# Kernel optimization log

Hardware: AMD Instinct MI355X
Metric: run time of the kernel (lower is better)

The kernel has to match this reference:

```python
import jax, jax.numpy as jnp
import numpy as np

B, C, H, W = 8, 64, 64, 64
CQ = C // 8  # query/key channels


def setup_inputs() -> dict:
    key = jax.random.key(0)
    ks = jax.random.split(key, 7)
    s = 0.05
    return {
        "x": jax.random.normal(ks[0], (B, C, H, W), jnp.float32),
        "wq": jax.random.normal(ks[1], (CQ, C), jnp.float32) * s,
        "bq": jnp.zeros((CQ,), jnp.float32),
        "wk": jax.random.normal(ks[2], (CQ, C), jnp.float32) * s,
        "bk": jnp.zeros((CQ,), jnp.float32),
        "wv": jax.random.normal(ks[3], (C, C), jnp.float32) * s,
        "bv": jnp.zeros((C,), jnp.float32),
    }


def reference(x, wq, bq, wk, bk, wv, bv):
    b, c, h, w = x.shape
    n = h * w
    xf = x.reshape(b, c, n)                       # [B, C, N]
    # 1x1 convs == per-pixel linear over channels
    q = jnp.einsum('oc,bcn->bon', wq, xf) + bq[None, :, None]   # [B, CQ, N]
    k = jnp.einsum('oc,bcn->bon', wk, xf) + bk[None, :, None]   # [B, CQ, N]
    v = jnp.einsum('oc,bcn->bon', wv, xf) + bv[None, :, None]   # [B, C, N]
    # energy[b, i, j] = q[b, :, i] . k[b, :, j]  (unscaled)
    energy = jnp.einsum('bci,bcj->bij', q, k)     # [B, N, N]
    attention = jax.nn.softmax(energy, axis=-1)   # softmax over j
    # out[b, c, i] = sum_j v[b, c, j] * attention[b, i, j]
    out = jnp.einsum('bcj,bij->bci', v, attention)
    return out.reshape(b, c, h, w)
```

## Files before the change

### kernel.cpp

```cpp
#include <hip/hip_runtime.h>
#include <hip/hip_bf16.h>


#define B_   8
#define C_   64
#define N_   4096
#define LOG2E 1.44269504088896340736f

typedef short bf16x8 __attribute__((ext_vector_type(8)));
typedef float f32x4  __attribute__((ext_vector_type(4)));
typedef unsigned int uint32;

#if __has_builtin(__builtin_amdgcn_exp2f)
#define EXP2(x) __builtin_amdgcn_exp2f(x)
#else
#define EXP2(x) __expf((x) * 0.69314718055994530942f)
#endif

__device__ __forceinline__ unsigned short f2bf_rn(float f) {
    union { __hip_bfloat16 h; unsigned short u; } cv;
    cv.h = __float2bfloat16(f);
    return cv.u;
}
__device__ __forceinline__ uint32 pk_rn(float lo, float hi) {
    return (uint32)f2bf_rn(lo) | ((uint32)f2bf_rn(hi) << 16);
}
__device__ __forceinline__ uint32 pack_rtz(float lo, float hi) {
    return __builtin_amdgcn_perm(__float_as_uint(hi), __float_as_uint(lo), 0x07060302);
}

__global__ __launch_bounds__(256) void prep_kernel(
    const float* __restrict__ x,
    const float* __restrict__ wq, const float* __restrict__ bq,
    const float* __restrict__ wk, const float* __restrict__ bk,
    unsigned short* __restrict__ Qh, unsigned short* __restrict__ Kh,
    unsigned short* __restrict__ Xb)
{
    __shared__ float Xs[C_][64];
    __shared__ float Wqk[16][C_];
    __shared__ float Bqk[16];

    const int t  = threadIdx.x;
    const int b  = blockIdx.x >> 6;
    const int p0 = (blockIdx.x & 63) << 6;

    for (int i = t; i < 1024; i += 256) {
        int o = i >> 6;
        Wqk[o][i & 63] = (o < 8) ? wq[i] * LOG2E : wk[i - 512];
    }
    if (t < 16) Bqk[t] = (t < 8) ? bq[t] * LOG2E : bk[t - 8];

    for (int i = t; i < 2048; i += 256) {
        int c = i >> 5, p2 = (i & 31) << 1;
        const float* xp = x + ((size_t)b * C_ + c) * N_ + p0 + p2;
        float2 v = *(const float2*)xp;
        Xs[c][p2] = v.x; Xs[c][p2 + 1] = v.y;
        *(uint32*)(Xb + ((size_t)b * C_ + c) * N_ + p0 + p2) = pk_rn(v.x, v.y);
    }
    __syncthreads();

    const int pix = t & 63, grp = t >> 6;
    float a[4];
    #pragma unroll
    for (int r = 0; r < 4; ++r) a[r] = Bqk[grp * 4 + r];
    for (int c = 0; c < C_; ++c) {
        float xv = Xs[c][pix];
        #pragma unroll
        for (int r = 0; r < 4; ++r) a[r] += Wqk[grp * 4 + r][c] * xv;
    }
    #pragma unroll
    for (int r = 0; r < 4; ++r) {
        int o = grp * 4 + r;
        unsigned short hv = f2bf_rn(a[r]);
        if (o < 8) Qh[((size_t)b * N_ + p0 + pix) * 8 + o] = hv;
        else       Kh[((size_t)b * N_ + p0 + pix) * 8 + (o - 8)] = hv;
    }
}

__global__ __launch_bounds__(256) void attn_mfma3_kernel(
    const unsigned short* __restrict__ Qh,
    const unsigned short* __restrict__ Kh,
    const unsigned short* __restrict__ Xb,
    const float* __restrict__ wv, const float* __restrict__ bv,
    float* __restrict__ out)
{
    __shared__ __align__(16) char smem[66560];

    const int t    = threadIdx.x;
    const int w    = t >> 6;
    const int lane = t & 63;
    const int l16  = lane & 15;
    const int qd   = lane >> 4;
    const int b    = blockIdx.x >> 6;
    const int i0   = (blockIdx.x & 63) << 6;

    const bf16x8 z8 = {};
    const f32x4  zf = {};

    bf16x8 qf[4];
    #pragma unroll
    for (int qt = 0; qt < 4; ++qt) {
        qf[qt] = z8;
        if (qd == 0)
            qf[qt] = *(const bf16x8*)(Qh + ((size_t)b * N_ + i0 + qt * 16 + l16) * 8);
    }

    const unsigned short* Kp = Kh + ((size_t)b * N_ + w * 1024) * 8;
    const unsigned short* Xp = Xb + (size_t)b * C_ * N_ + w * 1024;

    f32x4 acc[4][4];
    #pragma unroll
    for (int ct = 0; ct < 4; ++ct)
        #pragma unroll
        for (int qt = 0; qt < 4; ++qt) acc[ct][qt] = zf;
    float dsum[4] = {0.f, 0.f, 0.f, 0.f};

    const int swz   = (l16 & 3) << 2;
    const int wbase = w * 4096 + l16 * 64;
    int woff[2];
    #pragma unroll
    for (int jt = 0; jt < 2; ++jt) woff[jt] = ((jt * 8 + qd * 2) ^ swz) << 2;
    const int roff = ((qd * 4) ^ swz) << 2;

    bf16x8 kf[2][2], xf[2][4];
    #pragma unroll
    for (int jt = 0; jt < 2; ++jt) {
        kf[0][jt] = z8;
        if (qd == 0) kf[0][jt] = *(const bf16x8*)(Kp + (jt * 16 + l16) * 8);
    }
    #pragma unroll
    for (int ct = 0; ct < 4; ++ct)
        xf[0][ct] = *(const bf16x8*)(Xp + (size_t)(ct * 16 + l16) * N_ + qd * 8);

    #pragma unroll 2
    for (int s = 0; s < 32; ++s) {
        const int cur = s & 1, nxt = cur ^ 1;
        const int jb = s * 32;

        f32x4 sf[2][4];
        #pragma unroll
        for (int jt = 0; jt < 2; ++jt)
            #pragma unroll
            for (int qt = 0; qt < 4; ++qt)
                sf[jt][qt] = __builtin_amdgcn_mfma_f32_16x16x32_bf16(kf[cur][jt], qf[qt], zf, 0, 0, 0);

        if (s < 31) {
            #pragma unroll
            for (int jt = 0; jt < 2; ++jt) {
                bf16x8 nk = z8;
                if (qd == 0) nk = *(const bf16x8*)(Kp + (size_t)(jb + 32 + jt * 16 + l16) * 8);
                kf[nxt][jt] = nk;
            }
            #pragma unroll
            for (int ct = 0; ct < 4; ++ct)
                xf[nxt][ct] = *(const bf16x8*)(Xp + (size_t)(ct * 16 + l16) * N_ + jb + 32 + qd * 8);
        }

        #pragma unroll
        for (int jt = 0; jt < 2; ++jt)
            #pragma unroll
            for (int qt = 0; qt < 4; ++qt) {
                float e0 = EXP2(sf[jt][qt][0]);
                float e1 = EXP2(sf[jt][qt][1]);
                float e2 = EXP2(sf[jt][qt][2]);
                float e3 = EXP2(sf[jt][qt][3]);
                dsum[qt] += (e0 + e1) + (e2 + e3);
                uint2 u;
                u.x = pack_rtz(e0, e1);
                u.y = pack_rtz(e2, e3);
                *(uint2*)(smem + wbase + qt * 1024 + woff[jt]) = u;
            }

        #pragma unroll
        for (int qt = 0; qt < 4; ++qt) {
            bf16x8 pb = *(const bf16x8*)(smem + wbase + qt * 1024 + roff);
            #pragma unroll
            for (int ct = 0; ct < 4; ++ct)
                acc[ct][qt] = __builtin_amdgcn_mfma_f32_16x16x32_bf16(xf[cur][ct], pb, acc[ct][qt], 0, 0, 0);
        }
    }

    #pragma unroll
    for (int qt = 0; qt < 4; ++qt) {
        float v = dsum[qt];
        v += __shfl_xor(v, 16, 64);
        v += __shfl_xor(v, 32, 64);
        if (qd == 0) *(float*)(smem + 65536 + (w * 64 + qt * 16 + l16) * 4) = v;
    }
    if (w > 0) {
        char* rb = smem + 16384 + (w - 1) * 16384;
        #pragma unroll
        for (int ct = 0; ct < 4; ++ct)
            #pragma unroll
            for (int qt = 0; qt < 4; ++qt)
                *(f32x4*)(rb + (ct * 4 + qt) * 1024 + lane * 16) = acc[ct][qt];
    }
    __syncthreads();

    if (w == 0) {
        #pragma unroll
        for (int rr = 0; rr < 3; ++rr)
            #pragma unroll
            for (int ct = 0; ct < 4; ++ct)
                #pragma unroll
                for (int qt = 0; qt < 4; ++qt) {
                    f32x4 p = *(const f32x4*)(smem + 16384 + rr * 16384 + (ct * 4 + qt) * 1024 + lane * 16);
                    acc[ct][qt] += p;
                }
        float* Or = (float*)(smem + 16384);
        #pragma unroll
        for (int ct = 0; ct < 4; ++ct)
            #pragma unroll
            for (int qt = 0; qt < 4; ++qt)
                #pragma unroll
                for (int r = 0; r < 4; ++r)
                    Or[(ct * 16 + qd * 4 + r) * 64 + qt * 16 + l16] = acc[ct][qt][r];
    } else {
        float* Wvs = (float*)smem;
        for (int i = t - 64; i < 4096; i += 192) Wvs[i] = wv[i];
    }
    __syncthreads();

    const int q = t & 63, grp = t >> 6;
    const float* Wvs = (const float*)smem;
    const float* Or  = (const float*)(smem + 16384);
    const float* Dn  = (const float*)(smem + 65536);
    const float inv = 1.0f / (Dn[q] + Dn[64 + q] + Dn[128 + q] + Dn[192 + q]);
    float o[16];
    #pragma unroll
    for (int r = 0; r < 16; ++r) o[r] = 0.f;
    for (int k = 0; k < 64; ++k) {
        float ov = Or[k * 64 + q];
        #pragma unroll
        for (int r = 0; r < 16; ++r)
            o[r] += Wvs[(grp * 16 + r) * 64 + k] * ov;
    }
    #pragma unroll
    for (int r = 0; r < 16; ++r)
        out[((size_t)b * C_ + grp * 16 + r) * N_ + i0 + q] = o[r] * inv + bv[grp * 16 + r];
}

__global__ __launch_bounds__(256) void attn_fused_fallback(
    const float* __restrict__ x,
    const float* __restrict__ wq, const float* __restrict__ bq,
    const float* __restrict__ wk, const float* __restrict__ bk,
    const float* __restrict__ wv, const float* __restrict__ bv,
    float* __restrict__ out)
{
    __shared__ float Qs[64][8];
    __shared__ float Ks[8][64];
    __shared__ float Vs[64][C_];
    __shared__ float Ws[64][64 + 1];
    __shared__ float Xs[C_ * 64];
    __shared__ float Wks[8][C_];
    __shared__ float Wvs[C_][C_ + 1];

    const int t     = threadIdx.x;
    const int b     = blockIdx.x / (N_ / 64);
    const int i0    = (blockIdx.x % (N_ / 64)) * 64;
    const int jlane = t & 63;
    const int wgrp  = t >> 6;

    for (int l = t; l < 8 * C_;  l += 256) Wks[l >> 6][l & 63] = wk[l];
    for (int l = t; l < C_ * C_; l += 256) Wvs[l >> 6][l & 63] = wv[l];
    for (int l = t; l < C_ * 64; l += 256)
        Xs[(l >> 6) * 64 + (l & 63)] = x[((size_t)b * C_ + (l >> 6)) * N_ + i0 + (l & 63)];
    __syncthreads();
    {
        int qi = jlane;
        #pragma unroll
        for (int r = 0; r < 2; ++r) {
            int cc = wgrp * 2 + r;
            float a = bq[cc];
            for (int c = 0; c < C_; ++c) a += wq[cc * C_ + c] * Xs[c * 64 + qi];
            Qs[qi][cc] = a;
        }
    }
    __syncthreads();

    const int qi2 = t >> 2;
    const int cb  = (t & 3) << 4;
    float accv[16];
    #pragma unroll
    for (int r = 0; r < 16; ++r) accv[r] = 0.f;
    float denom = 0.f;

    for (int j0 = 0; j0 < N_; j0 += 64) {
        for (int l = t; l < C_ * 64; l += 256)
            Xs[(l >> 6) * 64 + (l & 63)] = x[((size_t)b * C_ + (l >> 6)) * N_ + j0 + (l & 63)];
        __syncthreads();
        {
            int j = jlane;
            #pragma unroll
            for (int r = 0; r < 2; ++r) {
                int cc = wgrp * 2 + r;
                float a = bk[cc];
                for (int c = 0; c < C_; ++c) a += Wks[cc][c] * Xs[c * 64 + j];
                Ks[cc][j] = a;
            }
        }
        {
            int vc = jlane;
            #pragma unroll 2
            for (int r = 0; r < 16; ++r) {
                int j = wgrp * 16 + r;
                float a = bv[vc];
                for (int c = 0; c < C_; ++c) a += Wvs[vc][c] * Xs[c * 64 + j];
                Vs[j][vc] = a;
            }
        }
        __syncthreads();
        {
            float kreg[8];
            #pragma unroll
            for (int cc = 0; cc < 8; ++cc) kreg[cc] = Ks[cc][jlane];
            #pragma unroll 4
            for (int r = 0; r < 16; ++r) {
                int qi = wgrp * 16 + r;
                float e = 0.f;
                #pragma unroll
                for (int cc = 0; cc < 8; ++cc) e += Qs[qi][cc] * kreg[cc];
                Ws[qi][jlane] = __expf(e);
            }
        }
        __syncthreads();
        #pragma unroll 4
        for (int j = 0; j < 64; ++j) {
            float wv2 = Ws[qi2][j];
            denom += wv2;
            const float4* vrow = (const float4*)(&Vs[j][cb]);
            float4 v0 = vrow[0], v1 = vrow[1], v2 = vrow[2], v3 = vrow[3];
            accv[0]  += wv2 * v0.x; accv[1]  += wv2 * v0.y; accv[2]  += wv2 * v0.z; accv[3]  += wv2 * v0.w;
            accv[4]  += wv2 * v1.x; accv[5]  += wv2 * v1.y; accv[6]  += wv2 * v1.z; accv[7]  += wv2 * v1.w;
            accv[8]  += wv2 * v2.x; accv[9]  += wv2 * v2.y; accv[10] += wv2 * v2.z; accv[11] += wv2 * v2.w;
            accv[12] += wv2 * v3.x; accv[13] += wv2 * v3.y; accv[14] += wv2 * v3.z; accv[15] += wv2 * v3.w;
        }
        __syncthreads();
    }

    const float inv = 1.0f / denom;
    #pragma unroll
    for (int r = 0; r < 16; ++r)
        out[((size_t)b * C_ + cb + r) * N_ + i0 + qi2] = accv[r] * inv;
}

extern "C" void kernel_launch(void* const* d_in, const int* in_sizes, int n_in,
                              void* d_out, int out_size, void* d_ws, size_t ws_size,
                              hipStream_t stream)
{
    const float* x  = (const float*)d_in[0];
    const float* wq = (const float*)d_in[1];
    const float* bq = (const float*)d_in[2];
    const float* wk = (const float*)d_in[3];
    const float* bk = (const float*)d_in[4];
    const float* wv = (const float*)d_in[5];
    const float* bv = (const float*)d_in[6];
    float* out = (float*)d_out;

    const size_t nQ = (size_t)B_ * N_ * 8;
    const size_t nX = (size_t)B_ * C_ * N_;
    const size_t needed = (2 * nQ + nX) * sizeof(unsigned short);

    if (ws_size >= needed) {
        unsigned short* Qh = (unsigned short*)d_ws;
        unsigned short* Kh = Qh + nQ;
        unsigned short* Xb = Kh + nQ;
        prep_kernel<<<B_ * (N_ / 64), 256, 0, stream>>>(x, wq, bq, wk, bk, Qh, Kh, Xb);
        attn_mfma3_kernel<<<B_ * (N_ / 64), 256, 0, stream>>>(Qh, Kh, Xb, wv, bv, out);
    } else {
        attn_fused_fallback<<<B_ * (N_ / 64), 256, 0, stream>>>(x, wq, bq, wk, bk, wv, bv, out);
    }
}
```

Baseline: 127.7 us.

## Halve query tile per block to double grid and raise occupancy

Each attention block now handles 32 query rows instead of 64, so the grid doubles from 512 to 1024 blocks and per-block shared memory shrinks from about 65KB to 25KB. Launch bounds now request 4 blocks per CU. The cross-wave reduction of partial outputs becomes a two-step tree through a smaller shared buffer, and the P-tile rows are padded to 80 bytes to cut bank conflicts. In exchange, every K/X tile is streamed twice as often per query and there are more barriers in the epilogue.

```diff
diff --git a/kernel.cpp b/kernel.cpp
--- a/kernel.cpp
+++ b/kernel.cpp
@@ -77,29 +77,29 @@
     }
 }
 
-__global__ __launch_bounds__(256) void attn_mfma3_kernel(
+__global__ __launch_bounds__(256, 4) void attn_mfma4_kernel(
     const unsigned short* __restrict__ Qh,
     const unsigned short* __restrict__ Kh,
     const unsigned short* __restrict__ Xb,
     const float* __restrict__ wv, const float* __restrict__ bv,
     float* __restrict__ out)
 {
-    __shared__ __align__(16) char smem[66560];
+    __shared__ __align__(16) char smem[25600];
 
     const int t    = threadIdx.x;
     const int w    = t >> 6;
     const int lane = t & 63;
     const int l16  = lane & 15;
     const int qd   = lane >> 4;
-    const int b    = blockIdx.x >> 6;
-    const int i0   = (blockIdx.x & 63) << 6;
+    const int b    = blockIdx.x >> 7;
+    const int i0   = (blockIdx.x & 127) << 5;
 
     const bf16x8 z8 = {};
     const f32x4  zf = {};
 
-    bf16x8 qf[4];
-    #pragma unroll
-    for (int qt = 0; qt < 4; ++qt) {
+    bf16x8 qf[2];
+    #pragma unroll
+    for (int qt = 0; qt < 2; ++qt) {
         qf[qt] = z8;
         if (qd == 0)
             qf[qt] = *(const bf16x8*)(Qh + ((size_t)b * N_ + i0 + qt * 16 + l16) * 8);
@@ -108,15 +108,15 @@
     const unsigned short* Kp = Kh + ((size_t)b * N_ + w * 1024) * 8;
     const unsigned short* Xp = Xb + (size_t)b * C_ * N_ + w * 1024;
 
-    f32x4 acc[4][4];
+    f32x4 acc[4][2];
     #pragma unroll
     for (int ct = 0; ct < 4; ++ct)
         #pragma unroll
-        for (int qt = 0; qt < 4; ++qt) acc[ct][qt] = zf;
-    float dsum[4] = {0.f, 0.f, 0.f, 0.f};
+        for (int qt = 0; qt < 2; ++qt) acc[ct][qt] = zf;
+    float dsum[2] = {0.f, 0.f};
 
     const int swz   = (l16 & 3) << 2;
-    const int wbase = w * 4096 + l16 * 64;
+    const int wbase = w * 2560 + l16 * 80;
     int woff[2];
     #pragma unroll
     for (int jt = 0; jt < 2; ++jt) woff[jt] = ((jt * 8 + qd * 2) ^ swz) << 2;
@@ -137,11 +137,11 @@
         const int cur = s & 1, nxt = cur ^ 1;
         const int jb = s * 32;
 
-        f32x4 sf[2][4];
+        f32x4 sf[2][2];
         #pragma unroll
         for (int jt = 0; jt < 2; ++jt)
             #pragma unroll
-            for (int qt = 0; qt < 4; ++qt)
+            for (int qt = 0; qt < 2; ++qt)
                 sf[jt][qt] = __builtin_amdgcn_mfma_f32_16x16x32_bf16(kf[cur][jt], qf[qt], zf, 0, 0, 0);
 
         if (s < 31) {
@@ -159,7 +159,7 @@
         #pragma unroll
         for (int jt = 0; jt < 2; ++jt)
             #pragma unroll
-            for (int qt = 0; qt < 4; ++qt) {
+            for (int qt = 0; qt < 2; ++qt) {
                 float e0 = EXP2(sf[jt][qt][0]);
                 float e1 = EXP2(sf[jt][qt][1]);
                 float e2 = EXP2(sf[jt][qt][2]);
@@ -168,12 +168,12 @@
                 uint2 u;
                 u.x = pack_rtz(e0, e1);
                 u.y = pack_rtz(e2, e3);
-                *(uint2*)(smem + wbase + qt * 1024 + woff[jt]) = u;
-            }
-
-        #pragma unroll
-        for (int qt = 0; qt < 4; ++qt) {
-            bf16x8 pb = *(const bf16x8*)(smem + wbase + qt * 1024 + roff);
+                *(uint2*)(smem + wbase + qt * 1280 + woff[jt]) = u;
+            }
+
+        #pragma unroll
+        for (int qt = 0; qt < 2; ++qt) {
+            bf16x8 pb = *(const bf16x8*)(smem + wbase + qt * 1280 + roff);
             #pragma unroll
             for (int ct = 0; ct < 4; ++ct)
                 acc[ct][qt] = __builtin_amdgcn_mfma_f32_16x16x32_bf16(xf[cur][ct], pb, acc[ct][qt], 0, 0, 0);
@@ -181,63 +181,80 @@
     }
 
     #pragma unroll
-    for (int qt = 0; qt < 4; ++qt) {
+    for (int qt = 0; qt < 2; ++qt) {
         float v = dsum[qt];
         v += __shfl_xor(v, 16, 64);
         v += __shfl_xor(v, 32, 64);
-        if (qd == 0) *(float*)(smem + 65536 + (w * 64 + qt * 16 + l16) * 4) = v;
-    }
-    if (w > 0) {
-        char* rb = smem + 16384 + (w - 1) * 16384;
-        #pragma unroll
-        for (int ct = 0; ct < 4; ++ct)
-            #pragma unroll
-            for (int qt = 0; qt < 4; ++qt)
-                *(f32x4*)(rb + (ct * 4 + qt) * 1024 + lane * 16) = acc[ct][qt];
-    }
-    __syncthreads();
-
+        if (qd == 0) *(float*)(smem + 24576 + (w * 32 + qt * 16 + l16) * 4) = v;
+    }
+
+    __syncthreads();
+    if (w >= 2) {
+        char* rb = smem + (w - 2) * 8192;
+        #pragma unroll
+        for (int ct = 0; ct < 4; ++ct)
+            #pragma unroll
+            for (int qt = 0; qt < 2; ++qt)
+                *(f32x4*)(rb + (ct * 2 + qt) * 1024 + lane * 16) = acc[ct][qt];
+    }
+    __syncthreads();
+    if (w < 2) {
+        const char* rb = smem + w * 8192;
+        #pragma unroll
+        for (int ct = 0; ct < 4; ++ct)
+            #pragma unroll
+            for (int qt = 0; qt < 2; ++qt)
+                acc[ct][qt] += *(const f32x4*)(rb + (ct * 2 + qt) * 1024 + lane * 16);
+    }
+    __syncthreads();
+    if (w == 1) {
+        char* rb = smem;
+        #pragma unroll
+        for (int ct = 0; ct < 4; ++ct)
+            #pragma unroll
+            for (int qt = 0; qt < 2; ++qt)
+                *(f32x4*)(rb + (ct * 2 + qt) * 1024 + lane * 16) = acc[ct][qt];
+    }
+    __syncthreads();
     if (w == 0) {
         #pragma unroll
-        for (int rr = 0; rr < 3; ++rr)
-            #pragma unroll
-            for (int ct = 0; ct < 4; ++ct)
-                #pragma unroll
-                for (int qt = 0; qt < 4; ++qt) {
-                    f32x4 p = *(const f32x4*)(smem + 16384 + rr * 16384 + (ct * 4 + qt) * 1024 + lane * 16);
-                    acc[ct][qt] += p;
-                }
+        for (int ct = 0; ct < 4; ++ct)
+            #pragma unroll
+            for (int qt = 0; qt < 2; ++qt)
+                acc[ct][qt] += *(const f32x4*)(smem + (ct * 2 + qt) * 1024 + lane * 16);
         float* Or = (float*)(smem + 16384);
         #pragma unroll
         for (int ct = 0; ct < 4; ++ct)
             #pragma unroll
-            for (int qt = 0; qt < 4; ++qt)
+            for (int qt = 0; qt < 2; ++qt)
                 #pragma unroll
                 for (int r = 0; r < 4; ++r)
-                    Or[(ct * 16 + qd * 4 + r) * 64 + qt * 16 + l16] = acc[ct][qt][r];
-    } else {
+                    Or[(ct * 16 + qd * 4 + r) * 32 + qt * 16 + l16] = acc[ct][qt][r];
+    }
+    __syncthreads();
+    {
         float* Wvs = (float*)smem;
-        for (int i = t - 64; i < 4096; i += 192) Wvs[i] = wv[i];
-    }
-    __syncthreads();
-
-    const int q = t & 63, grp = t >> 6;
+        for (int i = t; i < 4096; i += 256) Wvs[i] = wv[i];
+    }
+    __syncthreads();
+
+    const int q = t & 31, grp = t >> 5;
     const float* Wvs = (const float*)smem;
     const float* Or  = (const float*)(smem + 16384);
-    const float* Dn  = (const float*)(smem + 65536);
-    const float inv = 1.0f / (Dn[q] + Dn[64 + q] + Dn[128 + q] + Dn[192 + q]);
-    float o[16];
-    #pragma unroll
-    for (int r = 0; r < 16; ++r) o[r] = 0.f;
+    const float* Dn  = (const float*)(smem + 24576);
+    const float inv = 1.0f / (Dn[q] + Dn[32 + q] + Dn[64 + q] + Dn[96 + q]);
+    float o[8];
+    #pragma unroll
+    for (int r = 0; r < 8; ++r) o[r] = 0.f;
     for (int k = 0; k < 64; ++k) {
-        float ov = Or[k * 64 + q];
-        #pragma unroll
-        for (int r = 0; r < 16; ++r)
-            o[r] += Wvs[(grp * 16 + r) * 64 + k] * ov;
-    }
-    #pragma unroll
-    for (int r = 0; r < 16; ++r)
-        out[((size_t)b * C_ + grp * 16 + r) * N_ + i0 + q] = o[r] * inv + bv[grp * 16 + r];
+        float ov = Or[k * 32 + q];
+        #pragma unroll
+        for (int r = 0; r < 8; ++r)
+            o[r] += Wvs[(grp * 8 + r) * 64 + k] * ov;
+    }
+    #pragma unroll
+    for (int r = 0; r < 8; ++r)
+        out[((size_t)b * C_ + grp * 8 + r) * N_ + i0 + q] = o[r] * inv + bv[grp * 8 + r];
 }
 
 __global__ __launch_bounds__(256) void attn_fused_fallback(
@@ -366,7 +383,7 @@
         unsigned short* Kh = Qh + nQ;
         unsigned short* Xb = Kh + nQ;
         prep_kernel<<<B_ * (N_ / 64), 256, 0, stream>>>(x, wq, bq, wk, bk, Qh, Kh, Xb);
-        attn_mfma3_kernel<<<B_ * (N_ / 64), 256, 0, stream>>>(Qh, Kh, Xb, wv, bv, out);
+        attn_mfma4_kernel<<<B_ * (N_ / 32), 256, 0, stream>>>(Qh, Kh, Xb, wv, bv, out);
     } else {
         attn_fused_fallback<<<B_ * (N_ / 64), 256, 0, stream>>>(x, wq, bq, wk, bk, wv, bv, out);
     }
```

Result: slower. 151.7 us (+18.8%).

## Split key range across eight waves with tree reduction of partial outputs

Applied to the files above, without the earlier changes.

The attention kernel now runs 512 threads per block, so each of eight waves handles 512 keys instead of four waves handling 1024. Partial accumulators are combined in two stages through shared memory (waves 4-7 into 0-3, then 1-3 into 0). The final Wv projection is spread over 8 groups of 8 channels, and the Wv load now overlaps the reduction. The aim is more wavefronts for latency hiding on a grid of only 512 blocks, at the cost of extra synchronisation, extra reduction traffic and more registers per CU.

```diff
diff --git a/kernel.cpp b/kernel.cpp
--- a/kernel.cpp
+++ b/kernel.cpp
@@ -77,14 +77,14 @@
     }
 }
 
-__global__ __launch_bounds__(256) void attn_mfma3_kernel(
+__global__ __launch_bounds__(512) void attn_mfma7_kernel(
     const unsigned short* __restrict__ Qh,
     const unsigned short* __restrict__ Kh,
     const unsigned short* __restrict__ Xb,
     const float* __restrict__ wv, const float* __restrict__ bv,
     float* __restrict__ out)
 {
-    __shared__ __align__(16) char smem[66560];
+    __shared__ __align__(16) char smem[67584];
 
     const int t    = threadIdx.x;
     const int w    = t >> 6;
@@ -105,8 +105,8 @@
             qf[qt] = *(const bf16x8*)(Qh + ((size_t)b * N_ + i0 + qt * 16 + l16) * 8);
     }
 
-    const unsigned short* Kp = Kh + ((size_t)b * N_ + w * 1024) * 8;
-    const unsigned short* Xp = Xb + (size_t)b * C_ * N_ + w * 1024;
+    const unsigned short* Kp = Kh + ((size_t)b * N_ + w * 512) * 8;
+    const unsigned short* Xp = Xb + (size_t)b * C_ * N_ + w * 512;
 
     f32x4 acc[4][4];
     #pragma unroll
@@ -133,7 +133,7 @@
         xf[0][ct] = *(const bf16x8*)(Xp + (size_t)(ct * 16 + l16) * N_ + qd * 8);
 
     #pragma unroll 2
-    for (int s = 0; s < 32; ++s) {
+    for (int s = 0; s < 16; ++s) {
         const int cur = s & 1, nxt = cur ^ 1;
         const int jb = s * 32;
 
@@ -144,7 +144,7 @@
             for (int qt = 0; qt < 4; ++qt)
                 sf[jt][qt] = __builtin_amdgcn_mfma_f32_16x16x32_bf16(kf[cur][jt], qf[qt], zf, 0, 0, 0);
 
-        if (s < 31) {
+        if (s < 15) {
             #pragma unroll
             for (int jt = 0; jt < 2; ++jt) {
                 bf16x8 nk = z8;
@@ -187,8 +187,10 @@
         v += __shfl_xor(v, 32, 64);
         if (qd == 0) *(float*)(smem + 65536 + (w * 64 + qt * 16 + l16) * 4) = v;
     }
-    if (w > 0) {
-        char* rb = smem + 16384 + (w - 1) * 16384;
+
+    __syncthreads();
+    if (w >= 4) {
+        char* rb = smem + (w - 4) * 16384;
         #pragma unroll
         for (int ct = 0; ct < 4; ++ct)
             #pragma unroll
@@ -196,15 +198,36 @@
                 *(f32x4*)(rb + (ct * 4 + qt) * 1024 + lane * 16) = acc[ct][qt];
     }
     __syncthreads();
-
+    if (w < 4) {
+        const char* rb = smem + w * 16384;
+        #pragma unroll
+        for (int ct = 0; ct < 4; ++ct)
+            #pragma unroll
+            for (int qt = 0; qt < 4; ++qt)
+                acc[ct][qt] += *(const f32x4*)(rb + (ct * 4 + qt) * 1024 + lane * 16);
+    }
+    __syncthreads();
+    if (w >= 1 && w < 4) {
+        char* rb = smem + w * 16384;
+        #pragma unroll
+        for (int ct = 0; ct < 4; ++ct)
+            #pragma unroll
+            for (int qt = 0; qt < 4; ++qt)
+                *(f32x4*)(rb + (ct * 4 + qt) * 1024 + lane * 16) = acc[ct][qt];
+    }
+    if (w >= 4) {
+        float* Wvs = (float*)smem;
+        for (int i = t - 256; i < 4096; i += 256) Wvs[i] = wv[i];
+    }
+    __syncthreads();
     if (w == 0) {
         #pragma unroll
-        for (int rr = 0; rr < 3; ++rr)
+        for (int rr = 1; rr < 4; ++rr)
             #pragma unroll
             for (int ct = 0; ct < 4; ++ct)
                 #pragma unroll
                 for (int qt = 0; qt < 4; ++qt) {
-                    f32x4 p = *(const f32x4*)(smem + 16384 + rr * 16384 + (ct * 4 + qt) * 1024 + lane * 16);
+                    f32x4 p = *(const f32x4*)(smem + rr * 16384 + (ct * 4 + qt) * 1024 + lane * 16);
                     acc[ct][qt] += p;
                 }
         float* Or = (float*)(smem + 16384);
@@ -215,9 +238,6 @@
                 #pragma unroll
                 for (int r = 0; r < 4; ++r)
                     Or[(ct * 16 + qd * 4 + r) * 64 + qt * 16 + l16] = acc[ct][qt][r];
-    } else {
-        float* Wvs = (float*)smem;
-        for (int i = t - 64; i < 4096; i += 192) Wvs[i] = wv[i];
     }
     __syncthreads();
 
@@ -225,19 +245,22 @@
     const float* Wvs = (const float*)smem;
     const float* Or  = (const float*)(smem + 16384);
     const float* Dn  = (const float*)(smem + 65536);
-    const float inv = 1.0f / (Dn[q] + Dn[64 + q] + Dn[128 + q] + Dn[192 + q]);
-    float o[16];
-    #pragma unroll
-    for (int r = 0; r < 16; ++r) o[r] = 0.f;
+    float dtot = 0.f;
+    #pragma unroll
+    for (int r = 0; r < 8; ++r) dtot += Dn[r * 64 + q];
+    const float inv = 1.0f / dtot;
+    float o[8];
+    #pragma unroll
+    for (int r = 0; r < 8; ++r) o[r] = 0.f;
     for (int k = 0; k < 64; ++k) {
         float ov = Or[k * 64 + q];
         #pragma unroll
-        for (int r = 0; r < 16; ++r)
-            o[r] += Wvs[(grp * 16 + r) * 64 + k] * ov;
-    }
-    #pragma unroll
-    for (int r = 0; r < 16; ++r)
-        out[((size_t)b * C_ + grp * 16 + r) * N_ + i0 + q] = o[r] * inv + bv[grp * 16 + r];
+        for (int r = 0; r < 8; ++r)
+            o[r] += Wvs[(grp * 8 + r) * 64 + k] * ov;
+    }
+    #pragma unroll
+    for (int r = 0; r < 8; ++r)
+        out[((size_t)b * C_ + grp * 8 + r) * N_ + i0 + q] = o[r] * inv + bv[grp * 8 + r];
 }
 
 __global__ __launch_bounds__(256) void attn_fused_fallback(
@@ -366,7 +389,7 @@
         unsigned short* Kh = Qh + nQ;
         unsigned short* Xb = Kh + nQ;
         prep_kernel<<<B_ * (N_ / 64), 256, 0, stream>>>(x, wq, bq, wk, bk, Qh, Kh, Xb);
-        attn_mfma3_kernel<<<B_ * (N_ / 64), 256, 0, stream>>>(Qh, Kh, Xb, wv, bv, out);
+        attn_mfma7_kernel<<<B_ * (N_ / 64), 512, 0, stream>>>(Qh, Kh, Xb, wv, bv, out);
     } else {
         attn_fused_fallback<<<B_ * (N_ / 64), 256, 0, stream>>>(x, wq, bq, wk, bk, wv, bv, out);
     }
```

Result: slower. 132.0 us (+3.4%).
